# Performance work log

Measured on AMD Instinct MI355X. Metric: run time of the kernel, lower is better.

Reference implementation:

```python
import jax, jax.numpy as jnp
import numpy as np

ALPHA = 0.2  # LeakyReLU negative slope
EPS = 1e-16


def setup_inputs() -> dict:
    key = jax.random.key(0)
    k0, k1, k2, k3 = jax.random.split(key, 4)
    N, E, F_in, F_out, HEADS = 50000, 1600000, 256, 128, 4
    H = jax.random.normal(k0, (N, F_in), dtype=jnp.float32)
    edge_index = jax.random.randint(k1, (2, E), 0, N)  # row0=src, row1=dst
    # Xavier-ish scaled params
    W = jax.random.normal(k2, (HEADS, F_out, F_in), dtype=jnp.float32) * (1.0 / np.sqrt(F_in))
    a = jax.random.normal(k3, (HEADS, 2 * F_out), dtype=jnp.float32) * 0.1
    bias = jnp.zeros((F_out,), dtype=jnp.float32)
    return {"H": H, "edge_index": edge_index, "W": W, "a": a, "bias": bias}


def reference(H, edge_index, W, a, bias):
    """GAT layer: per-head edge attention + segment softmax over src + SpMM, mean over heads.

    H: [N, F_in]; edge_index: [2, E]; W: [heads, F_out, F_in]; a: [heads, 2*F_out]; bias: [F_out]
    Note: a(concat(h_src, h_dst)) == h_src @ a[:F_out] + h_dst @ a[F_out:], so we compute the
    two per-node scores once on nodes instead of materializing the E x 2*F_out concat.
    """
    N = H.shape[0]
    heads, F_out, _ = W.shape
    src, dst = edge_index[0], edge_index[1]
    outs = []
    for h in range(heads):
        Ht = H @ W[h].T                      # [N, F_out]
        s_src = Ht @ a[h, :F_out]            # [N]
        s_dst = Ht @ a[h, F_out:]            # [N]
        e = s_src[src] + s_dst[dst]          # [E]
        e = jnp.where(e > 0, e, ALPHA * e)   # LeakyReLU
        # segment softmax over src nodes (matches scatter amax + scatter_add)
        e_max = jax.ops.segment_max(e, src, num_segments=N)    # [N], -inf for isolated nodes
        e_exp = jnp.exp(e - e_max[src])                         # [E]
        denom = jax.ops.segment_sum(e_exp, src, num_segments=N) # [N]
        attn = e_exp / (denom[src] + EPS)                       # [E]
        # sparse.mm(attention, Ht): out[i] = sum_{(i,j) in E} attn_ij * Ht[j]
        out = jax.ops.segment_sum(attn[:, None] * Ht[dst], src, num_segments=N)  # [N, F_out]
        outs.append(out)
    final = jnp.mean(jnp.stack(outs, axis=0), axis=0) + bias
    return final
```

## Files before the change

kernel.cpp:

```cpp
#include <hip/hip_runtime.h>

#define ALPHA 0.2f
#define EPS 1e-16f

static constexpr int F_IN = 256;
static constexpr int F_OUT = 128;
static constexpr int HEADS = 4;
static constexpr int COLS = HEADS * F_OUT;

typedef __bf16 bf16x8 __attribute__((ext_vector_type(8)));
typedef float f32x4 __attribute__((ext_vector_type(4)));

static __device__ __forceinline__ unsigned short f2bf(float f) {
  unsigned int u = __float_as_uint(f);
  unsigned int r = (u + 0x7FFFu + ((u >> 16) & 1u)) >> 16;
  return (unsigned short)r;
}
static __device__ __forceinline__ float bf_lo(unsigned int u) {
  return __uint_as_float(u << 16);
}
static __device__ __forceinline__ float bf_hi(unsigned int u) {
  return __uint_as_float(u & 0xFFFF0000u);
}

__global__ __launch_bounds__(256) void k_gemm_q(const float* __restrict__ A,
                                                const float* __restrict__ Wf,
                                                unsigned char* __restrict__ Hq,
                                                unsigned char* __restrict__ rec,
                                                float* __restrict__ ssrc,
                                                const float* __restrict__ Av, int N, int Tg,
                                                const int* __restrict__ src,
                                                int* __restrict__ cnt,
                                                unsigned short* __restrict__ rank, int E) {
  if ((int)blockIdx.x >= Tg) {
    int i = ((int)blockIdx.x - Tg) * 256 + threadIdx.x;
    const int stride = 1024 * 256;
    for (; i < E; i += stride) rank[i] = (unsigned short)atomicAdd(&cnt[src[i]], 1);
    return;
  }
  __shared__ __bf16 As[128][40];
  __shared__ __bf16 Bs[128][40];
  __shared__ float sS[128], sD[128];
  const int T = Tg;
  const int q8 = T >> 3, r8 = T & 7;
  const int xcd = blockIdx.x & 7, ii = blockIdx.x >> 3;
  const int gp = (xcd < r8) ? xcd * (q8 + 1) + ii
                            : r8 * (q8 + 1) + (xcd - r8) * q8 + ii;
  const int by = gp >> 2;
  const int bx = gp & 3;
  const int t = threadIdx.x;
  const int w = t >> 6, l = t & 63;
  const int wr = w >> 1, wc = w & 1;
  const int m0 = by << 7, n0 = bx << 7;
  const int lr = t >> 1, seg16 = (t & 1) << 4;
  f32x4 acc[4][4] = {};
  for (int k0 = 0; k0 < F_IN; k0 += 32) {
    int ar = m0 + lr; if (ar >= N) ar = N - 1;
    const float4 f0 = *(const float4*)&A[(size_t)ar * F_IN + k0 + seg16];
    const float4 f1 = *(const float4*)&A[(size_t)ar * F_IN + k0 + seg16 + 4];
    const float4 f2 = *(const float4*)&A[(size_t)ar * F_IN + k0 + seg16 + 8];
    const float4 f3 = *(const float4*)&A[(size_t)ar * F_IN + k0 + seg16 + 12];
    const float4 g0 = *(const float4*)&Wf[(size_t)(n0 + lr) * F_IN + k0 + seg16];
    const float4 g1 = *(const float4*)&Wf[(size_t)(n0 + lr) * F_IN + k0 + seg16 + 4];
    const float4 g2 = *(const float4*)&Wf[(size_t)(n0 + lr) * F_IN + k0 + seg16 + 8];
    const float4 g3 = *(const float4*)&Wf[(size_t)(n0 + lr) * F_IN + k0 + seg16 + 12];
    bf16x8 v0, v1, u0, u1;
    v0[0] = (__bf16)f0.x; v0[1] = (__bf16)f0.y; v0[2] = (__bf16)f0.z; v0[3] = (__bf16)f0.w;
    v0[4] = (__bf16)f1.x; v0[5] = (__bf16)f1.y; v0[6] = (__bf16)f1.z; v0[7] = (__bf16)f1.w;
    v1[0] = (__bf16)f2.x; v1[1] = (__bf16)f2.y; v1[2] = (__bf16)f2.z; v1[3] = (__bf16)f2.w;
    v1[4] = (__bf16)f3.x; v1[5] = (__bf16)f3.y; v1[6] = (__bf16)f3.z; v1[7] = (__bf16)f3.w;
    u0[0] = (__bf16)g0.x; u0[1] = (__bf16)g0.y; u0[2] = (__bf16)g0.z; u0[3] = (__bf16)g0.w;
    u0[4] = (__bf16)g1.x; u0[5] = (__bf16)g1.y; u0[6] = (__bf16)g1.z; u0[7] = (__bf16)g1.w;
    u1[0] = (__bf16)g2.x; u1[1] = (__bf16)g2.y; u1[2] = (__bf16)g2.z; u1[3] = (__bf16)g2.w;
    u1[4] = (__bf16)g3.x; u1[5] = (__bf16)g3.y; u1[6] = (__bf16)g3.z; u1[7] = (__bf16)g3.w;
    __syncthreads();
    *(bf16x8*)&As[lr][seg16] = v0;  *(bf16x8*)&As[lr][seg16 + 8] = v1;
    *(bf16x8*)&Bs[lr][seg16] = u0;  *(bf16x8*)&Bs[lr][seg16 + 8] = u1;
    __syncthreads();
    const int kb = (l >> 4) << 3;
    bf16x8 af[4], bf_[4];
#pragma unroll
    for (int mi = 0; mi < 4; ++mi)
      af[mi] = *(const bf16x8*)&As[(wr << 6) + (mi << 4) + (l & 15)][kb];
#pragma unroll
    for (int ni = 0; ni < 4; ++ni)
      bf_[ni] = *(const bf16x8*)&Bs[(wc << 6) + (ni << 4) + (l & 15)][kb];
#pragma unroll
    for (int mi = 0; mi < 4; ++mi)
#pragma unroll
      for (int ni = 0; ni < 4; ++ni)
        acc[mi][ni] = __builtin_amdgcn_mfma_f32_16x16x32_bf16(af[mi], bf_[ni], acc[mi][ni], 0, 0, 0);
  }
  {
    float as_[4], ad_[4];
#pragma unroll
    for (int ni = 0; ni < 4; ++ni) {
      const int f = (wc << 6) + (ni << 4) + (l & 15);
      as_[ni] = Av[bx * 256 + f];
      ad_[ni] = Av[bx * 256 + 128 + f];
    }
#pragma unroll
    for (int mi = 0; mi < 4; ++mi)
#pragma unroll
      for (int r = 0; r < 4; ++r) {
        float ds_ = 0.f, dd_ = 0.f;
#pragma unroll
        for (int ni = 0; ni < 4; ++ni) {
          ds_ = fmaf(acc[mi][ni][r], as_[ni], ds_);
          dd_ = fmaf(acc[mi][ni][r], ad_[ni], dd_);
        }
#pragma unroll
        for (int m = 1; m < 16; m <<= 1) {
          ds_ += __shfl_xor(ds_, m);
          dd_ += __shfl_xor(dd_, m);
        }
        if (wc == 0 && (l & 15) == 0) {
          const int rl = (wr << 6) + (mi << 4) + ((l >> 4) << 2) + r;
          sS[rl] = ds_; sD[rl] = dd_;
        }
      }
    __syncthreads();
    if (wc == 1) {
#pragma unroll
      for (int mi = 0; mi < 4; ++mi)
#pragma unroll
        for (int r = 0; r < 4; ++r) {
          float ds_ = 0.f, dd_ = 0.f;
#pragma unroll
          for (int ni = 0; ni < 4; ++ni) {
            ds_ = fmaf(acc[mi][ni][r], as_[ni], ds_);
            dd_ = fmaf(acc[mi][ni][r], ad_[ni], dd_);
          }
#pragma unroll
          for (int m = 1; m < 16; m <<= 1) {
            ds_ += __shfl_xor(ds_, m);
            dd_ += __shfl_xor(dd_, m);
          }
          if ((l & 15) == 0) {
            const int rl = (wr << 6) + (mi << 4) + ((l >> 4) << 2) + r;
            const int row = m0 + rl;
            if (row < N) {
              ssrc[row * 4 + bx] = sS[rl] + ds_;
              *(float*)&rec[(size_t)row * 32 + (bx << 2)] = sD[rl] + dd_;
            }
          }
        }
    }
  }
  const int bxg = (bx << 1) + wc;
#pragma unroll
  for (int mi = 0; mi < 4; ++mi)
#pragma unroll
    for (int r = 0; r < 4; ++r) {
      float mx = 0.f;
#pragma unroll
      for (int ni = 0; ni < 4; ++ni) mx = fmaxf(mx, fabsf(acc[mi][ni][r]));
#pragma unroll
      for (int m = 1; m < 16; m <<= 1) mx = fmaxf(mx, __shfl_xor(mx, m));
      const int row = m0 + (wr << 6) + (mi << 4) + ((l >> 4) << 2) + r;
      if (row < N) {
        const float inv = (mx > 0.f) ? 127.f / mx : 0.f;
        if ((l & 15) == 0)
          *(unsigned short*)&rec[(size_t)row * 32 + 16 + (bxg << 1)] = f2bf(mx * (1.f / 127.f));
        unsigned int pk = 0;
#pragma unroll
        for (int ni = 0; ni < 4; ++ni) {
          float tq = fminf(fmaxf(rintf(acc[mi][ni][r] * inv), -127.f), 127.f);
          pk |= ((unsigned int)(((int)tq + 128) & 255)) << (8 * ni);
        }
        *(unsigned int*)&Hq[(size_t)row * 512 + (bxg << 6) + ((l & 15) << 2)] = pk;
      }
    }
}

__global__ __launch_bounds__(1024) void k_scan1(int* __restrict__ cnt,
                                                int* __restrict__ bsum, int N) {
  __shared__ int ws[16];
  const int t = threadIdx.x, g = blockIdx.x * 1024 + t;
  const int lane = t & 63, w = t >> 6;
  int v = (g < N) ? cnt[g] : 0;
#pragma unroll
  for (int o = 1; o < 64; o <<= 1) {
    const int y = __shfl_up(v, o);
    if (lane >= o) v += y;
  }
  if (lane == 63) ws[w] = v;
  __syncthreads();
  if (w == 0) {
    int s = (lane < 16) ? ws[lane] : 0;
#pragma unroll
    for (int o = 1; o < 16; o <<= 1) {
      const int y = __shfl_up(s, o);
      if (lane >= o) s += y;
    }
    if (lane < 16) ws[lane] = s;
  }
  __syncthreads();
  v += (w > 0) ? ws[w - 1] : 0;
  if (g < N) cnt[g] = v;
  if (t == 1023) bsum[blockIdx.x] = v;
}

__global__ __launch_bounds__(1024) void k_scan3(const int* __restrict__ part,
                                                const int* __restrict__ bsum,
                                                int* __restrict__ off, int N, int nb) {
  __shared__ int sbuf[256];
  const int t = threadIdx.x;
  if (t < 64) {
    int carry = 0;
    for (int base = 0; base < nb; base += 64) {
      int v = (base + t < nb) ? bsum[base + t] : 0;
#pragma unroll
      for (int o = 1; o < 64; o <<= 1) {
        const int y = __shfl_up(v, o);
        if (t >= o) v += y;
      }
      v += carry;
      if (base + t < nb) sbuf[base + t] = v;
      carry = __shfl(v, 63);
    }
  }
  __syncthreads();
  const int g = blockIdx.x * 1024 + t;
  if (g == 0) off[0] = 0;
  if (g < N) off[g + 1] = part[g] + (blockIdx.x ? sbuf[blockIdx.x - 1] : 0);
}

__global__ void k_scatter(const int* __restrict__ src, const int* __restrict__ dst,
                          const int* __restrict__ off, const unsigned short* __restrict__ rank,
                          unsigned short* __restrict__ csr_dst, int E) {
  int i = blockIdx.x * blockDim.x + threadIdx.x;
  const int stride = gridDim.x * blockDim.x;
  for (; i < E; i += stride)
    csr_dst[off[src[i]] + rank[i]] = (unsigned short)dst[i];
}

__global__ __launch_bounds__(256) void k_spmm(const uint2* __restrict__ Hq2,
    const float4* __restrict__ ssrc4, const unsigned char* __restrict__ rec,
    const int* __restrict__ off, const unsigned short* __restrict__ csr_dst,
    const float* __restrict__ bias, float* __restrict__ out, int N) {
  __shared__ float wbuf[4][8][72];
  __shared__ int   ibuf[4][64];
  const int wv = threadIdx.x >> 6;
  const int lane = threadIdx.x & 63;
  const int n = (blockIdx.x << 2) + wv;
  if (n >= N) return;
  const int hg = lane >> 4;
  const int b8 = lane >> 3;
  const float4 ss4 = ssrc4[n];
  float den4[4] = {};
  float acc[8] = {};
  float sw = 0.f;
  const int beg = off[n], end = off[n + 1];
  for (int c0 = beg; c0 < end; c0 += 64) {
    const int cnt = min(64, end - c0);
    if (lane < cnt) {
      const int d = csr_dst[c0 + lane];
      ibuf[wv][lane] = d << 6;
      const float4 sd4 = *(const float4*)&rec[(size_t)d * 32];
      const uint4  sc  = *(const uint4*)&rec[(size_t)d * 32 + 16];
      float e0 = ss4.x + sd4.x; e0 = fmaxf(e0, ALPHA * e0);
      float e1 = ss4.y + sd4.y; e1 = fmaxf(e1, ALPHA * e1);
      float e2 = ss4.z + sd4.z; e2 = fmaxf(e2, ALPHA * e2);
      float e3 = ss4.w + sd4.w; e3 = fmaxf(e3, ALPHA * e3);
      const float w0 = __expf(e0), w1 = __expf(e1), w2 = __expf(e2), w3 = __expf(e3);
      den4[0] += w0; den4[1] += w1; den4[2] += w2; den4[3] += w3;
      wbuf[wv][0][lane] = w0 * bf_lo(sc.x); wbuf[wv][1][lane] = w0 * bf_hi(sc.x);
      wbuf[wv][2][lane] = w1 * bf_lo(sc.y); wbuf[wv][3][lane] = w1 * bf_hi(sc.y);
      wbuf[wv][4][lane] = w2 * bf_lo(sc.z); wbuf[wv][5][lane] = w2 * bf_hi(sc.z);
      wbuf[wv][6][lane] = w3 * bf_lo(sc.w); wbuf[wv][7][lane] = w3 * bf_hi(sc.w);
    }
#pragma unroll 8
    for (int j = 0; j < cnt; ++j) {
      const float wgt = wbuf[wv][b8][j];
      const int db = ibuf[wv][j];
      const uint2 q = Hq2[db + lane];
      sw += wgt;
      acc[0] = fmaf(wgt, (float)(q.x & 0xffu),         acc[0]);
      acc[1] = fmaf(wgt, (float)((q.x >> 8) & 0xffu),  acc[1]);
      acc[2] = fmaf(wgt, (float)((q.x >> 16) & 0xffu), acc[2]);
      acc[3] = fmaf(wgt, (float)(q.x >> 24),           acc[3]);
      acc[4] = fmaf(wgt, (float)(q.y & 0xffu),         acc[4]);
      acc[5] = fmaf(wgt, (float)((q.y >> 8) & 0xffu),  acc[5]);
      acc[6] = fmaf(wgt, (float)((q.y >> 16) & 0xffu), acc[6]);
      acc[7] = fmaf(wgt, (float)(q.y >> 24),           acc[7]);
    }
  }
#pragma unroll
  for (int k = 0; k < 4; ++k)
#pragma unroll
    for (int m = 1; m < 64; m <<= 1) den4[k] += __shfl_xor(den4[k], m);
  const float r = 1.f / (den4[hg] + EPS);
  const float corr = 128.f * sw;
#pragma unroll
  for (int i = 0; i < 8; ++i) acc[i] = (acc[i] - corr) * r;
#pragma unroll
  for (int i = 0; i < 8; ++i) {
    acc[i] += __shfl_xor(acc[i], 16);
    acc[i] += __shfl_xor(acc[i], 32);
  }
  if (lane < 16) {
    const int base = ((lane >> 3) & 1) * 64 + ((lane & 7) << 1);
#pragma unroll
    for (int k = 0; k < 4; ++k) {
      const float2 b2 = *(const float2*)&bias[base + k * 16];
      *(float2*)&out[(size_t)n * F_OUT + base + k * 16] =
          make_float2(0.25f * acc[k] + b2.x, 0.25f * acc[k + 4] + b2.y);
    }
  }
}

extern "C" void kernel_launch(void* const* d_in, const int* in_sizes, int n_in,
                              void* d_out, int out_size, void* d_ws, size_t ws_size,
                              hipStream_t stream) {
  const float* H    = (const float*)d_in[0];
  const int*   ei   = (const int*)d_in[1];
  const float* W    = (const float*)d_in[2];
  const float* a    = (const float*)d_in[3];
  const float* bias = (const float*)d_in[4];
  const int N = in_sizes[0] / F_IN;
  const int E = in_sizes[1] / 2;
  const int* src = ei;
  const int* dst = ei + E;

  char* ws = (char*)d_ws;
  size_t o = 0;
  auto alloc = [&](size_t bytes) -> void* {
    void* p = ws + o;
    o = (o + bytes + 255) & ~(size_t)255;
    return p;
  };
  unsigned char*  Hq  = (unsigned char*)alloc((size_t)N * COLS);
  float* ssrc = (float*)alloc((size_t)N * HEADS * sizeof(float));
  unsigned char* rec = (unsigned char*)alloc((size_t)N * 32);
  int*   cnt  = (int*)alloc((size_t)N * sizeof(int));
  int*   off  = (int*)alloc(((size_t)N + 1) * sizeof(int));
  unsigned short* csr = (unsigned short*)alloc((size_t)E * sizeof(unsigned short));
  unsigned short* rank = (unsigned short*)alloc((size_t)E * sizeof(unsigned short));
  const int nb = (N + 1023) / 1024;
  int*   bsum = (int*)alloc((size_t)nb * sizeof(int));

  hipMemsetAsync(cnt, 0, (size_t)N * sizeof(int), stream);

  const int nb128 = (N + 127) / 128;
  const int Tg = 4 * nb128;
  k_gemm_q<<<Tg + 1024, 256, 0, stream>>>(H, W, Hq, rec, ssrc, a, N, Tg,
                                          src, cnt, rank, E);
  k_scan1<<<nb, 1024, 0, stream>>>(cnt, bsum, N);
  k_scan3<<<nb, 1024, 0, stream>>>(cnt, bsum, off, N, nb);
  k_scatter<<<1024, 256, 0, stream>>>(src, dst, off, rank, csr, E);
  k_spmm<<<(N + 3) / 4, 256, 0, stream>>>((const uint2*)Hq, (const float4*)ssrc,
                                          rec, off, csr, bias, (float*)d_out, N);
}
```

Measured before the change: 289.6 us.

## Load GEMM fragments directly from global memory, dropping LDS staging and barriers

The projection GEMM no longer stages A and W tiles through shared memory. Each lane now loads its MFMA fragments straight from global memory and converts them to bf16 in registers, which removes the LDS writes, LDS reads and both __syncthreads per k-step. Launch bounds now request 2 blocks per CU. The cost is redundant global loads: each A row is read by both column-waves and each W row by both row-waves, so the kernel leans on L1/L2 hits. The per-lane 32-byte strided accesses are also less coalesced.

```diff
diff --git a/kernel.cpp b/kernel.cpp
--- a/kernel.cpp
+++ b/kernel.cpp
@@ -23,23 +23,21 @@
   return __uint_as_float(u & 0xFFFF0000u);
 }
 
-__global__ __launch_bounds__(256) void k_gemm_q(const float* __restrict__ A,
-                                                const float* __restrict__ Wf,
-                                                unsigned char* __restrict__ Hq,
-                                                unsigned char* __restrict__ rec,
-                                                float* __restrict__ ssrc,
-                                                const float* __restrict__ Av, int N, int Tg,
-                                                const int* __restrict__ src,
-                                                int* __restrict__ cnt,
-                                                unsigned short* __restrict__ rank, int E) {
+__global__ __launch_bounds__(256, 2) void k_gemm_q(const float* __restrict__ A,
+                                                   const float* __restrict__ Wf,
+                                                   unsigned char* __restrict__ Hq,
+                                                   unsigned char* __restrict__ rec,
+                                                   float* __restrict__ ssrc,
+                                                   const float* __restrict__ Av, int N, int Tg,
+                                                   const int* __restrict__ src,
+                                                   int* __restrict__ cnt,
+                                                   unsigned short* __restrict__ rank, int E) {
   if ((int)blockIdx.x >= Tg) {
     int i = ((int)blockIdx.x - Tg) * 256 + threadIdx.x;
     const int stride = 1024 * 256;
     for (; i < E; i += stride) rank[i] = (unsigned short)atomicAdd(&cnt[src[i]], 1);
     return;
   }
-  __shared__ __bf16 As[128][40];
-  __shared__ __bf16 Bs[128][40];
   __shared__ float sS[128], sD[128];
   const int T = Tg;
   const int q8 = T >> 3, r8 = T & 7;
@@ -52,39 +50,41 @@
   const int w = t >> 6, l = t & 63;
   const int wr = w >> 1, wc = w & 1;
   const int m0 = by << 7, n0 = bx << 7;
-  const int lr = t >> 1, seg16 = (t & 1) << 4;
+  const int lrow = l & 15;
+  const int kq = (l >> 4) << 3;
+  const float* arow[4];
+  const float* wrow[4];
+#pragma unroll
+  for (int mi = 0; mi < 4; ++mi) {
+    int r = m0 + (wr << 6) + (mi << 4) + lrow;
+    if (r >= N) r = N - 1;
+    arow[mi] = A + (size_t)r * F_IN + kq;
+  }
+#pragma unroll
+  for (int ni = 0; ni < 4; ++ni)
+    wrow[ni] = Wf + (size_t)(n0 + (wc << 6) + (ni << 4) + lrow) * F_IN + kq;
+
   f32x4 acc[4][4] = {};
   for (int k0 = 0; k0 < F_IN; k0 += 32) {
-    int ar = m0 + lr; if (ar >= N) ar = N - 1;
-    const float4 f0 = *(const float4*)&A[(size_t)ar * F_IN + k0 + seg16];
-    const float4 f1 = *(const float4*)&A[(size_t)ar * F_IN + k0 + seg16 + 4];
-    const float4 f2 = *(const float4*)&A[(size_t)ar * F_IN + k0 + seg16 + 8];
-    const float4 f3 = *(const float4*)&A[(size_t)ar * F_IN + k0 + seg16 + 12];
-    const float4 g0 = *(const float4*)&Wf[(size_t)(n0 + lr) * F_IN + k0 + seg16];
-    const float4 g1 = *(const float4*)&Wf[(size_t)(n0 + lr) * F_IN + k0 + seg16 + 4];
-    const float4 g2 = *(const float4*)&Wf[(size_t)(n0 + lr) * F_IN + k0 + seg16 + 8];
-    const float4 g3 = *(const float4*)&Wf[(size_t)(n0 + lr) * F_IN + k0 + seg16 + 12];
-    bf16x8 v0, v1, u0, u1;
-    v0[0] = (__bf16)f0.x; v0[1] = (__bf16)f0.y; v0[2] = (__bf16)f0.z; v0[3] = (__bf16)f0.w;
-    v0[4] = (__bf16)f1.x; v0[5] = (__bf16)f1.y; v0[6] = (__bf16)f1.z; v0[7] = (__bf16)f1.w;
-    v1[0] = (__bf16)f2.x; v1[1] = (__bf16)f2.y; v1[2] = (__bf16)f2.z; v1[3] = (__bf16)f2.w;
-    v1[4] = (__bf16)f3.x; v1[5] = (__bf16)f3.y; v1[6] = (__bf16)f3.z; v1[7] = (__bf16)f3.w;
-    u0[0] = (__bf16)g0.x; u0[1] = (__bf16)g0.y; u0[2] = (__bf16)g0.z; u0[3] = (__bf16)g0.w;
-    u0[4] = (__bf16)g1.x; u0[5] = (__bf16)g1.y; u0[6] = (__bf16)g1.z; u0[7] = (__bf16)g1.w;
-    u1[0] = (__bf16)g2.x; u1[1] = (__bf16)g2.y; u1[2] = (__bf16)g2.z; u1[3] = (__bf16)g2.w;
-    u1[4] = (__bf16)g3.x; u1[5] = (__bf16)g3.y; u1[6] = (__bf16)g3.z; u1[7] = (__bf16)g3.w;
-    __syncthreads();
-    *(bf16x8*)&As[lr][seg16] = v0;  *(bf16x8*)&As[lr][seg16 + 8] = v1;
-    *(bf16x8*)&Bs[lr][seg16] = u0;  *(bf16x8*)&Bs[lr][seg16 + 8] = u1;
-    __syncthreads();
-    const int kb = (l >> 4) << 3;
     bf16x8 af[4], bf_[4];
 #pragma unroll
-    for (int mi = 0; mi < 4; ++mi)
-      af[mi] = *(const bf16x8*)&As[(wr << 6) + (mi << 4) + (l & 15)][kb];
-#pragma unroll
-    for (int ni = 0; ni < 4; ++ni)
-      bf_[ni] = *(const bf16x8*)&Bs[(wc << 6) + (ni << 4) + (l & 15)][kb];
+    for (int mi = 0; mi < 4; ++mi) {
+      const float4 p0 = *(const float4*)(arow[mi] + k0);
+      const float4 p1 = *(const float4*)(arow[mi] + k0 + 4);
+      af[mi][0] = (__bf16)p0.x; af[mi][1] = (__bf16)p0.y;
+      af[mi][2] = (__bf16)p0.z; af[mi][3] = (__bf16)p0.w;
+      af[mi][4] = (__bf16)p1.x; af[mi][5] = (__bf16)p1.y;
+      af[mi][6] = (__bf16)p1.z; af[mi][7] = (__bf16)p1.w;
+    }
+#pragma unroll
+    for (int ni = 0; ni < 4; ++ni) {
+      const float4 p0 = *(const float4*)(wrow[ni] + k0);
+      const float4 p1 = *(const float4*)(wrow[ni] + k0 + 4);
+      bf_[ni][0] = (__bf16)p0.x; bf_[ni][1] = (__bf16)p0.y;
+      bf_[ni][2] = (__bf16)p0.z; bf_[ni][3] = (__bf16)p0.w;
+      bf_[ni][4] = (__bf16)p1.x; bf_[ni][5] = (__bf16)p1.y;
+      bf_[ni][6] = (__bf16)p1.z; bf_[ni][7] = (__bf16)p1.w;
+    }
 #pragma unroll
     for (int mi = 0; mi < 4; ++mi)
 #pragma unroll
@@ -95,7 +95,7 @@
     float as_[4], ad_[4];
 #pragma unroll
     for (int ni = 0; ni < 4; ++ni) {
-      const int f = (wc << 6) + (ni << 4) + (l & 15);
+      const int f = (wc << 6) + (ni << 4) + lrow;
       as_[ni] = Av[bx * 256 + f];
       ad_[ni] = Av[bx * 256 + 128 + f];
     }
```

After: 353.0 us. +21.9%, slower.

## Double-buffer GEMM LDS tiles and launch atomic-count blocks before GEMM blocks

Applied to the files above, without the earlier changes.

The GEMM main loop now uses two shared-memory buffers: global loads for the next K-slice are issued before the MFMAs on the current slice and written to the alternate buffer afterwards, leaving one barrier per iteration instead of two. The edge-counting (atomic rank) blocks are moved to the front of the grid so they get dispatched first and overlap with the GEMM tiles. This doubles LDS use for the tile buffers, which may lower occupancy, and raises register pressure from holding the prefetched data.

```diff
diff --git a/kernel.cpp b/kernel.cpp
--- a/kernel.cpp
+++ b/kernel.cpp
@@ -21,6 +21,11 @@
 }
 static __device__ __forceinline__ float bf_hi(unsigned int u) {
   return __uint_as_float(u & 0xFFFF0000u);
+}
+
+static __device__ __forceinline__ void cvt8(const float4& p0, const float4& p1, bf16x8& v) {
+  v[0] = (__bf16)p0.x; v[1] = (__bf16)p0.y; v[2] = (__bf16)p0.z; v[3] = (__bf16)p0.w;
+  v[4] = (__bf16)p1.x; v[5] = (__bf16)p1.y; v[6] = (__bf16)p1.z; v[7] = (__bf16)p1.w;
 }
 
 __global__ __launch_bounds__(256) void k_gemm_q(const float* __restrict__ A,
@@ -32,18 +37,18 @@
                                                 const int* __restrict__ src,
                                                 int* __restrict__ cnt,
                                                 unsigned short* __restrict__ rank, int E) {
-  if ((int)blockIdx.x >= Tg) {
-    int i = ((int)blockIdx.x - Tg) * 256 + threadIdx.x;
+  if ((int)blockIdx.x < 1024) {
+    int i = (int)blockIdx.x * 256 + threadIdx.x;
     const int stride = 1024 * 256;
     for (; i < E; i += stride) rank[i] = (unsigned short)atomicAdd(&cnt[src[i]], 1);
     return;
   }
-  __shared__ __bf16 As[128][40];
-  __shared__ __bf16 Bs[128][40];
+  __shared__ __bf16 As[2][128][40];
+  __shared__ __bf16 Bs[2][128][40];
   __shared__ float sS[128], sD[128];
-  const int T = Tg;
-  const int q8 = T >> 3, r8 = T & 7;
-  const int xcd = blockIdx.x & 7, ii = blockIdx.x >> 3;
+  const int gb = (int)blockIdx.x - 1024;
+  const int q8 = Tg >> 3, r8 = Tg & 7;
+  const int xcd = gb & 7, ii = gb >> 3;
   const int gp = (xcd < r8) ? xcd * (q8 + 1) + ii
                             : r8 * (q8 + 1) + (xcd - r8) * q8 + ii;
   const int by = gp >> 2;
@@ -53,43 +58,61 @@
   const int wr = w >> 1, wc = w & 1;
   const int m0 = by << 7, n0 = bx << 7;
   const int lr = t >> 1, seg16 = (t & 1) << 4;
+  int ar = m0 + lr; if (ar >= N) ar = N - 1;
+  const float* Ap = A + (size_t)ar * F_IN + seg16;
+  const float* Wp = Wf + (size_t)(n0 + lr) * F_IN + seg16;
+
   f32x4 acc[4][4] = {};
-  for (int k0 = 0; k0 < F_IN; k0 += 32) {
-    int ar = m0 + lr; if (ar >= N) ar = N - 1;
-    const float4 f0 = *(const float4*)&A[(size_t)ar * F_IN + k0 + seg16];
-    const float4 f1 = *(const float4*)&A[(size_t)ar * F_IN + k0 + seg16 + 4];
-    const float4 f2 = *(const float4*)&A[(size_t)ar * F_IN + k0 + seg16 + 8];
-    const float4 f3 = *(const float4*)&A[(size_t)ar * F_IN + k0 + seg16 + 12];
-    const float4 g0 = *(const float4*)&Wf[(size_t)(n0 + lr) * F_IN + k0 + seg16];
-    const float4 g1 = *(const float4*)&Wf[(size_t)(n0 + lr) * F_IN + k0 + seg16 + 4];
-    const float4 g2 = *(const float4*)&Wf[(size_t)(n0 + lr) * F_IN + k0 + seg16 + 8];
-    const float4 g3 = *(const float4*)&Wf[(size_t)(n0 + lr) * F_IN + k0 + seg16 + 12];
+  {
+    const float4 f0 = *(const float4*)(Ap + 0);
+    const float4 f1 = *(const float4*)(Ap + 4);
+    const float4 f2 = *(const float4*)(Ap + 8);
+    const float4 f3 = *(const float4*)(Ap + 12);
+    const float4 g0 = *(const float4*)(Wp + 0);
+    const float4 g1 = *(const float4*)(Wp + 4);
+    const float4 g2 = *(const float4*)(Wp + 8);
+    const float4 g3 = *(const float4*)(Wp + 12);
     bf16x8 v0, v1, u0, u1;
-    v0[0] = (__bf16)f0.x; v0[1] = (__bf16)f0.y; v0[2] = (__bf16)f0.z; v0[3] = (__bf16)f0.w;
-    v0[4] = (__bf16)f1.x; v0[5] = (__bf16)f1.y; v0[6] = (__bf16)f1.z; v0[7] = (__bf16)f1.w;
-    v1[0] = (__bf16)f2.x; v1[1] = (__bf16)f2.y; v1[2] = (__bf16)f2.z; v1[3] = (__bf16)f2.w;
-    v1[4] = (__bf16)f3.x; v1[5] = (__bf16)f3.y; v1[6] = (__bf16)f3.z; v1[7] = (__bf16)f3.w;
-    u0[0] = (__bf16)g0.x; u0[1] = (__bf16)g0.y; u0[2] = (__bf16)g0.z; u0[3] = (__bf16)g0.w;
-    u0[4] = (__bf16)g1.x; u0[5] = (__bf16)g1.y; u0[6] = (__bf16)g1.z; u0[7] = (__bf16)g1.w;
-    u1[0] = (__bf16)g2.x; u1[1] = (__bf16)g2.y; u1[2] = (__bf16)g2.z; u1[3] = (__bf16)g2.w;
-    u1[4] = (__bf16)g3.x; u1[5] = (__bf16)g3.y; u1[6] = (__bf16)g3.z; u1[7] = (__bf16)g3.w;
-    __syncthreads();
-    *(bf16x8*)&As[lr][seg16] = v0;  *(bf16x8*)&As[lr][seg16 + 8] = v1;
-    *(bf16x8*)&Bs[lr][seg16] = u0;  *(bf16x8*)&Bs[lr][seg16 + 8] = u1;
-    __syncthreads();
-    const int kb = (l >> 4) << 3;
+    cvt8(f0, f1, v0); cvt8(f2, f3, v1);
+    cvt8(g0, g1, u0); cvt8(g2, g3, u1);
+    *(bf16x8*)&As[0][lr][seg16] = v0;  *(bf16x8*)&As[0][lr][seg16 + 8] = v1;
+    *(bf16x8*)&Bs[0][lr][seg16] = u0;  *(bf16x8*)&Bs[0][lr][seg16 + 8] = u1;
+  }
+  __syncthreads();
+  const int kb = (l >> 4) << 3;
+  const int arow_f = (wr << 6) + (l & 15);
+  const int brow_f = (wc << 6) + (l & 15);
+#pragma unroll
+  for (int s = 0; s < 8; ++s) {
+    const int cur = s & 1;
+    float4 f0, f1, f2, f3, g0, g1, g2, g3;
+    if (s < 7) {
+      const int k0 = (s + 1) << 5;
+      f0 = *(const float4*)(Ap + k0);      f1 = *(const float4*)(Ap + k0 + 4);
+      f2 = *(const float4*)(Ap + k0 + 8);  f3 = *(const float4*)(Ap + k0 + 12);
+      g0 = *(const float4*)(Wp + k0);      g1 = *(const float4*)(Wp + k0 + 4);
+      g2 = *(const float4*)(Wp + k0 + 8);  g3 = *(const float4*)(Wp + k0 + 12);
+    }
     bf16x8 af[4], bf_[4];
 #pragma unroll
     for (int mi = 0; mi < 4; ++mi)
-      af[mi] = *(const bf16x8*)&As[(wr << 6) + (mi << 4) + (l & 15)][kb];
+      af[mi] = *(const bf16x8*)&As[cur][arow_f + (mi << 4)][kb];
 #pragma unroll
     for (int ni = 0; ni < 4; ++ni)
-      bf_[ni] = *(const bf16x8*)&Bs[(wc << 6) + (ni << 4) + (l & 15)][kb];
+      bf_[ni] = *(const bf16x8*)&Bs[cur][brow_f + (ni << 4)][kb];
 #pragma unroll
     for (int mi = 0; mi < 4; ++mi)
 #pragma unroll
       for (int ni = 0; ni < 4; ++ni)
         acc[mi][ni] = __builtin_amdgcn_mfma_f32_16x16x32_bf16(af[mi], bf_[ni], acc[mi][ni], 0, 0, 0);
+    if (s < 7) {
+      bf16x8 v0, v1, u0, u1;
+      cvt8(f0, f1, v0); cvt8(f2, f3, v1);
+      cvt8(g0, g1, u0); cvt8(g2, g3, u1);
+      *(bf16x8*)&As[cur ^ 1][lr][seg16] = v0;  *(bf16x8*)&As[cur ^ 1][lr][seg16 + 8] = v1;
+      *(bf16x8*)&Bs[cur ^ 1][lr][seg16] = u0;  *(bf16x8*)&Bs[cur ^ 1][lr][seg16 + 8] = u1;
+    }
+    __syncthreads();
   }
   {
     float as_[4], ad_[4];
@@ -344,7 +367,7 @@
 
   const int nb128 = (N + 127) / 128;
   const int Tg = 4 * nb128;
-  k_gemm_q<<<Tg + 1024, 256, 0, stream>>>(H, W, Hq, rec, ssrc, a, N, Tg,
+  k_gemm_q<<<1024 + Tg, 256, 0, stream>>>(H, W, Hq, rec, ssrc, a, N, Tg,
                                           src, cnt, rank, E);
   k_scan1<<<nb, 1024, 0, stream>>>(cnt, bsum, N);
   k_scan3<<<nb, 1024, 0, stream>>>(cnt, bsum, off, N, nb);
```

Result: slower. 304.0 us (+4.9%).

## Replace global-atomic CSR build with per-block LDS histogram counting sort

Applied to the files above, without the earlier changes.

Moves the edge-to-CSR construction off global atomics into a two-pass counting sort. Each of 256 blocks histograms its slice of edges in shared memory using packed 16-bit counters. Per-block counts are then column-summed and prefix-scanned, and a placement pass writes dst indices using those bases. The extra bcnt/base arrays add 2×256×N×2 bytes of traffic and three more kernel launches. The GEMM also stops co-hosting the rank-atomic blocks and hoists its row pointer math out of the loop.

```diff
diff --git a/kernel.cpp b/kernel.cpp
--- a/kernel.cpp
+++ b/kernel.cpp
@@ -7,6 +7,7 @@
 static constexpr int F_OUT = 128;
 static constexpr int HEADS = 4;
 static constexpr int COLS = HEADS * F_OUT;
+static constexpr int NB_SORT = 256;
 
 typedef __bf16 bf16x8 __attribute__((ext_vector_type(8)));
 typedef float f32x4 __attribute__((ext_vector_type(4)));
@@ -21,6 +22,75 @@
 }
 static __device__ __forceinline__ float bf_hi(unsigned int u) {
   return __uint_as_float(u & 0xFFFF0000u);
+}
+static __device__ __forceinline__ void cvt8(const float4& p0, const float4& p1, bf16x8& v) {
+  v[0] = (__bf16)p0.x; v[1] = (__bf16)p0.y; v[2] = (__bf16)p0.z; v[3] = (__bf16)p0.w;
+  v[4] = (__bf16)p1.x; v[5] = (__bf16)p1.y; v[6] = (__bf16)p1.z; v[7] = (__bf16)p1.w;
+}
+
+
+__global__ __launch_bounds__(256) void k_cnt(const int* __restrict__ src,
+                                             unsigned short* __restrict__ bcnt,
+                                             int N, int E) {
+  __shared__ unsigned int bins[25088];
+  const int b = blockIdx.x, t = threadIdx.x;
+  const int NBIN = (N + 1) >> 1;
+  for (int j = t; j < NBIN; j += 256) bins[j] = 0u;
+  __syncthreads();
+  const int CE = (E + NB_SORT - 1) / NB_SORT;
+  const int i1 = min(E, (b + 1) * CE);
+  for (int i = b * CE + t; i < i1; i += 256) {
+    const int s = src[i];
+    atomicAdd(&bins[s >> 1], 1u << ((s & 1) << 4));
+  }
+  __syncthreads();
+  unsigned short* row = bcnt + (size_t)b * N;
+  for (int s = t; s < N; s += 256)
+    row[s] = (unsigned short)((bins[s >> 1] >> ((s & 1) << 4)) & 0xffffu);
+}
+
+__global__ __launch_bounds__(1024) void k_colsum(const unsigned short* __restrict__ bcnt,
+                                                 int* __restrict__ cnt, int N) {
+  const int s = blockIdx.x * 1024 + threadIdx.x;
+  if (s >= N) return;
+  int run = 0;
+  for (int b = 0; b < NB_SORT; ++b) run += bcnt[(size_t)b * N + s];
+  cnt[s] = run;
+}
+
+__global__ __launch_bounds__(1024) void k_base(const unsigned short* __restrict__ bcnt,
+                                               unsigned short* __restrict__ base_rel, int N) {
+  const int s = blockIdx.x * 1024 + threadIdx.x;
+  if (s >= N) return;
+  int run = 0;
+  for (int b = 0; b < NB_SORT; ++b) {
+    const size_t idx = (size_t)b * N + s;
+    const int v = bcnt[idx];
+    base_rel[idx] = (unsigned short)run;
+    run += v;
+  }
+}
+
+__global__ __launch_bounds__(256) void k_place(const int* __restrict__ src,
+                                               const int* __restrict__ dst,
+                                               const int* __restrict__ off,
+                                               const unsigned short* __restrict__ base_rel,
+                                               unsigned short* __restrict__ csr,
+                                               int N, int E) {
+  __shared__ unsigned int bins[25088];
+  const int b = blockIdx.x, t = threadIdx.x;
+  const int NBIN = (N + 1) >> 1;
+  for (int j = t; j < NBIN; j += 256) bins[j] = 0u;
+  __syncthreads();
+  const unsigned short* brow = base_rel + (size_t)b * N;
+  const int CE = (E + NB_SORT - 1) / NB_SORT;
+  const int i1 = min(E, (b + 1) * CE);
+  for (int i = b * CE + t; i < i1; i += 256) {
+    const int s = src[i];
+    const unsigned int old = atomicAdd(&bins[s >> 1], 1u << ((s & 1) << 4));
+    const int local = (old >> ((s & 1) << 4)) & 0xffff;
+    csr[off[s] + brow[s] + local] = (unsigned short)dst[i];
+  }
 }
 
 __global__ __launch_bounds__(256) void k_gemm_q(const float* __restrict__ A,
@@ -28,21 +98,11 @@
                                                 unsigned char* __restrict__ Hq,
                                                 unsigned char* __restrict__ rec,
                                                 float* __restrict__ ssrc,
-                                                const float* __restrict__ Av, int N, int Tg,
-                                                const int* __restrict__ src,
-                                                int* __restrict__ cnt,
-                                                unsigned short* __restrict__ rank, int E) {
-  if ((int)blockIdx.x >= Tg) {
-    int i = ((int)blockIdx.x - Tg) * 256 + threadIdx.x;
-    const int stride = 1024 * 256;
-    for (; i < E; i += stride) rank[i] = (unsigned short)atomicAdd(&cnt[src[i]], 1);
-    return;
-  }
+                                                const float* __restrict__ Av, int N, int Tg) {
   __shared__ __bf16 As[128][40];
   __shared__ __bf16 Bs[128][40];
   __shared__ float sS[128], sD[128];
-  const int T = Tg;
-  const int q8 = T >> 3, r8 = T & 7;
+  const int q8 = Tg >> 3, r8 = Tg & 7;
   const int xcd = blockIdx.x & 7, ii = blockIdx.x >> 3;
   const int gp = (xcd < r8) ? xcd * (q8 + 1) + ii
                             : r8 * (q8 + 1) + (xcd - r8) * q8 + ii;
@@ -53,26 +113,22 @@
   const int wr = w >> 1, wc = w & 1;
   const int m0 = by << 7, n0 = bx << 7;
   const int lr = t >> 1, seg16 = (t & 1) << 4;
+  int ar = m0 + lr; if (ar >= N) ar = N - 1;
+  const float* Ap = A + (size_t)ar * F_IN + seg16;
+  const float* Wp = Wf + (size_t)(n0 + lr) * F_IN + seg16;
   f32x4 acc[4][4] = {};
   for (int k0 = 0; k0 < F_IN; k0 += 32) {
-    int ar = m0 + lr; if (ar >= N) ar = N - 1;
-    const float4 f0 = *(const float4*)&A[(size_t)ar * F_IN + k0 + seg16];
-    const float4 f1 = *(const float4*)&A[(size_t)ar * F_IN + k0 + seg16 + 4];
-    const float4 f2 = *(const float4*)&A[(size_t)ar * F_IN + k0 + seg16 + 8];
-    const float4 f3 = *(const float4*)&A[(size_t)ar * F_IN + k0 + seg16 + 12];
-    const float4 g0 = *(const float4*)&Wf[(size_t)(n0 + lr) * F_IN + k0 + seg16];
-    const float4 g1 = *(const float4*)&Wf[(size_t)(n0 + lr) * F_IN + k0 + seg16 + 4];
-    const float4 g2 = *(const float4*)&Wf[(size_t)(n0 + lr) * F_IN + k0 + seg16 + 8];
-    const float4 g3 = *(const float4*)&Wf[(size_t)(n0 + lr) * F_IN + k0 + seg16 + 12];
+    const float4 f0 = *(const float4*)(Ap + k0);
+    const float4 f1 = *(const float4*)(Ap + k0 + 4);
+    const float4 f2 = *(const float4*)(Ap + k0 + 8);
+    const float4 f3 = *(const float4*)(Ap + k0 + 12);
+    const float4 g0 = *(const float4*)(Wp + k0);
+    const float4 g1 = *(const float4*)(Wp + k0 + 4);
+    const float4 g2 = *(const float4*)(Wp + k0 + 8);
+    const float4 g3 = *(const float4*)(Wp + k0 + 12);
     bf16x8 v0, v1, u0, u1;
-    v0[0] = (__bf16)f0.x; v0[1] = (__bf16)f0.y; v0[2] = (__bf16)f0.z; v0[3] = (__bf16)f0.w;
-    v0[4] = (__bf16)f1.x; v0[5] = (__bf16)f1.y; v0[6] = (__bf16)f1.z; v0[7] = (__bf16)f1.w;
-    v1[0] = (__bf16)f2.x; v1[1] = (__bf16)f2.y; v1[2] = (__bf16)f2.z; v1[3] = (__bf16)f2.w;
-    v1[4] = (__bf16)f3.x; v1[5] = (__bf16)f3.y; v1[6] = (__bf16)f3.z; v1[7] = (__bf16)f3.w;
-    u0[0] = (__bf16)g0.x; u0[1] = (__bf16)g0.y; u0[2] = (__bf16)g0.z; u0[3] = (__bf16)g0.w;
-    u0[4] = (__bf16)g1.x; u0[5] = (__bf16)g1.y; u0[6] = (__bf16)g1.z; u0[7] = (__bf16)g1.w;
-    u1[0] = (__bf16)g2.x; u1[1] = (__bf16)g2.y; u1[2] = (__bf16)g2.z; u1[3] = (__bf16)g2.w;
-    u1[4] = (__bf16)g3.x; u1[5] = (__bf16)g3.y; u1[6] = (__bf16)g3.z; u1[7] = (__bf16)g3.w;
+    cvt8(f0, f1, v0); cvt8(f2, f3, v1);
+    cvt8(g0, g1, u0); cvt8(g2, g3, u1);
     __syncthreads();
     *(bf16x8*)&As[lr][seg16] = v0;  *(bf16x8*)&As[lr][seg16 + 8] = v1;
     *(bf16x8*)&Bs[lr][seg16] = u0;  *(bf16x8*)&Bs[lr][seg16 + 8] = u1;
@@ -224,15 +280,6 @@
   const int g = blockIdx.x * 1024 + t;
   if (g == 0) off[0] = 0;
   if (g < N) off[g + 1] = part[g] + (blockIdx.x ? sbuf[blockIdx.x - 1] : 0);
-}
-
-__global__ void k_scatter(const int* __restrict__ src, const int* __restrict__ dst,
-                          const int* __restrict__ off, const unsigned short* __restrict__ rank,
-                          unsigned short* __restrict__ csr_dst, int E) {
-  int i = blockIdx.x * blockDim.x + threadIdx.x;
-  const int stride = gridDim.x * blockDim.x;
-  for (; i < E; i += stride)
-    csr_dst[off[src[i]] + rank[i]] = (unsigned short)dst[i];
 }
 
 __global__ __launch_bounds__(256) void k_spmm(const uint2* __restrict__ Hq2,
@@ -335,20 +382,22 @@
   unsigned char* rec = (unsigned char*)alloc((size_t)N * 32);
   int*   cnt  = (int*)alloc((size_t)N * sizeof(int));
   int*   off  = (int*)alloc(((size_t)N + 1) * sizeof(int));
-  unsigned short* csr = (unsigned short*)alloc((size_t)E * sizeof(unsigned short));
-  unsigned short* rank = (unsigned short*)alloc((size_t)E * sizeof(unsigned short));
+  unsigned short* csr  = (unsigned short*)alloc((size_t)E * sizeof(unsigned short));
+  unsigned short* bcnt = (unsigned short*)alloc((size_t)NB_SORT * N * sizeof(unsigned short));
+  unsigned short* base = (unsigned short*)alloc((size_t)NB_SORT * N * sizeof(unsigned short));
   const int nb = (N + 1023) / 1024;
   int*   bsum = (int*)alloc((size_t)nb * sizeof(int));
 
-  hipMemsetAsync(cnt, 0, (size_t)N * sizeof(int), stream);
-
   const int nb128 = (N + 127) / 128;
   const int Tg = 4 * nb128;
-  k_gemm_q<<<Tg + 1024, 256, 0, stream>>>(H, W, Hq, rec, ssrc, a, N, Tg,
-                                          src, cnt, rank, E);
+
+  k_cnt<<<NB_SORT, 256, 0, stream>>>(src, bcnt, N, E);
+  k_gemm_q<<<Tg, 256, 0, stream>>>(H, W, Hq, rec, ssrc, a, N, Tg);
+  k_colsum<<<nb, 1024, 0, stream>>>(bcnt, cnt, N);
   k_scan1<<<nb, 1024, 0, stream>>>(cnt, bsum, N);
   k_scan3<<<nb, 1024, 0, stream>>>(cnt, bsum, off, N, nb);
-  k_scatter<<<1024, 256, 0, stream>>>(src, dst, off, rank, csr, E);
+  k_base<<<nb, 1024, 0, stream>>>(bcnt, base, N);
+  k_place<<<NB_SORT, 256, 0, stream>>>(src, dst, off, base, csr, N, E);
   k_spmm<<<(N + 3) / 4, 256, 0, stream>>>((const uint2*)Hq, (const float4*)ssrc,
                                           rec, off, csr, bias, (float*)d_out, N);
 }
```

Result: slower. 303.9 us (+4.9%).
